# Performance work log

Measured on AMD Instinct MI355X. Metric: run time of the kernel, lower is better.

The kernel has to match this reference:

```python
import jax, jax.numpy as jnp
import numpy as np

N = 100_000      # total nodes in batched graph
NE = 800_000     # total edges
G = 1_000        # number of graphs in batch
V_DIM = 128      # node feat dim (== H_DIM, required by GRUCell usage)
E_DIM = 64       # edge feat dim
H_DIM = 128      # hidden dim
K_HEAD = 4       # multi-scale interaction heads


def _leaky(x):
    return jnp.where(x >= 0, x, 0.1 * x)


def _gru_cell(x, h, Wih, Whh, bih, bhh):
    # torch nn.GRUCell math; Wih/Whh stored as [in, 3*h] with (r,z,n) chunk order
    gi = x @ Wih + bih
    gh = h @ Whh + bhh
    ir, iz, inn = jnp.split(gi, 3, axis=-1)
    hr, hz, hn = jnp.split(gh, 3, axis=-1)
    r = jax.nn.sigmoid(ir + hr)
    z = jax.nn.sigmoid(iz + hz)
    n = jnp.tanh(inn + r * hn)
    return (1.0 - z) * n + z * h


def setup_inputs() -> dict:
    key = jax.random.key(0)
    ks = iter(jax.random.split(key, 48))
    def rn(shape, scale=0.05):
        return (jax.random.normal(next(ks), shape) * scale).astype(jnp.float32)
    inp = {}
    inp["v"] = rn((N, V_DIM), 1.0)
    inp["e"] = rn((NE, E_DIM), 1.0)
    inp["s"] = rn((G, V_DIM), 1.0)
    inp["edge_src"] = jax.random.randint(next(ks), (NE,), 0, N)
    inp["edge_dst"] = jax.random.randint(next(ks), (NE,), 0, N)
    inp["node_graph"] = jnp.repeat(jnp.arange(G), N // G)  # sorted segment ids
    # top-level linears (stored [in, out])
    inp["A_w"] = rn((V_DIM, H_DIM)); inp["A_b"] = rn((H_DIM,))
    inp["mA_w"] = rn((K_HEAD, V_DIM, H_DIM)); inp["mA_b"] = rn((K_HEAD, H_DIM))
    inp["mB_w"] = rn((K_HEAD, V_DIM, H_DIM)); inp["mB_b"] = rn((K_HEAD, H_DIM))
    inp["mC_w"] = rn((K_HEAD, H_DIM)); inp["mC_b"] = rn((K_HEAD,))
    inp["mD_w"] = rn((K_HEAD, V_DIM, H_DIM)); inp["mD_b"] = rn((K_HEAD, H_DIM))
    inp["B_w"] = rn((H_DIM * K_HEAD, H_DIM)); inp["B_b"] = rn((H_DIM,))
    inp["C_w"] = rn((V_DIM, H_DIM)); inp["C_b"] = rn((H_DIM,))
    inp["K_w"] = rn((E_DIM, H_DIM)); inp["K_b"] = rn((H_DIM,))
    inp["E_w"] = rn((H_DIM + V_DIM, H_DIM)); inp["E_b"] = rn((H_DIM,))
    for pfx in ("gm", "gs"):
        inp[pfx + "_A_w"] = rn((H_DIM, H_DIM)); inp[pfx + "_A_b"] = rn((H_DIM,))
        inp[pfx + "_B_w"] = rn((H_DIM, H_DIM)); inp[pfx + "_B_b"] = rn((H_DIM,))
        inp[pfx + "_Wih"] = rn((H_DIM, 3 * H_DIM)); inp[pfx + "_Whh"] = rn((H_DIM, 3 * H_DIM))
        inp[pfx + "_bih"] = rn((3 * H_DIM,)); inp[pfx + "_bhh"] = rn((3 * H_DIM,))
    return inp


def reference(v, e, s, edge_src, edge_dst, node_graph,
              A_w, A_b, mA_w, mA_b, mB_w, mB_b, mC_w, mC_b, mD_w, mD_b,
              B_w, B_b, C_w, C_b, K_w, K_b, E_w, E_b,
              gm_A_w, gm_A_b, gm_B_w, gm_B_b, gm_Wih, gm_Whh, gm_bih, gm_bhh,
              gs_A_w, gs_A_b, gs_B_w, gs_B_b, gs_Wih, gs_Whh, gs_bih, gs_bhh):
    # super -> super
    s2s = jnp.tanh(s @ A_w + A_b)                                       # [G,H]
    # multi-head node->super attention pooling (Multi_scale_interaction)
    d_node = jnp.tanh(jnp.einsum('nv,kvh->knh', v, mA_w) + mA_b[:, None, :])     # [K,N,H]
    d_super = jnp.tanh(jnp.einsum('gv,kvh->kgh', s, mB_w) + mB_b[:, None, :])    # [K,G,H]
    a = jnp.einsum('knh,kh->nk', d_node * d_super[:, node_graph, :], mC_w) + mC_b[None, :]  # [N,K]
    a_max = jax.ops.segment_max(a, node_graph, num_segments=G, indices_are_sorted=True)
    a_exp = jnp.exp(a - a_max[node_graph])
    denom = jax.ops.segment_sum(a_exp, node_graph, num_segments=G, indices_are_sorted=True)
    attn = a_exp / denom[node_graph]                                    # per-graph softmax, [N,K]
    d_v = jnp.einsum('nv,kvh->nkh', v, mD_w) + mD_b[None, :, :]         # [N,K,H]
    pooled = jax.ops.segment_sum(d_v * attn[:, :, None], node_graph, num_segments=G,
                                 indices_are_sorted=True)               # [G,K,H]
    m2s = jnp.tanh(pooled.reshape(G, K_HEAD * H_DIM) @ B_w + B_b)       # [G,H]
    # super -> node broadcast
    s2m = jnp.tanh(s @ C_w + C_b)[node_graph]                           # [N,H]
    # edge-wise message: leaky_relu(K(e) * v_src) summed into destination node
    ve = _leaky((e @ K_w + K_b) * v[edge_src])                          # [E,H]
    sve = jax.ops.segment_sum(ve, edge_dst, num_segments=N)             # [N,H]
    m2m = _leaky(jnp.concatenate([sve, v], axis=1) @ E_w + E_b)         # [N,H]
    # adaptive GRU gate: node update
    z_m = jax.nn.sigmoid(m2m @ gm_A_w + gm_A_b + s2m @ gm_B_w + gm_B_b)
    h_m = z_m * s2m + (1.0 - z_m) * m2m
    update_v = _gru_cell(v, h_m, gm_Wih, gm_Whh, gm_bih, gm_bhh)
    # adaptive GRU gate: supernode update
    z_s = jax.nn.sigmoid(s2s @ gs_A_w + gs_A_b + m2s @ gs_B_w + gs_B_b)
    h_s = z_s * m2s + (1.0 - z_s) * s2s
    update_s = _gru_cell(s, h_s, gs_Wih, gs_Whh, gs_bih, gs_bhh)
    return (update_v, update_s)
```

## Files before the change

### kernel.cpp

```cpp
#include <hip/hip_runtime.h>

#define NN   100000
#define NEDG 800000
#define NG   1000
#define HD   128
#define EDIM 64

typedef unsigned short u16;
typedef __bf16 bf16x8 __attribute__((ext_vector_type(8)));
typedef float f32x4 __attribute__((ext_vector_type(4)));
typedef u16 u16x8 __attribute__((ext_vector_type(8)));
typedef unsigned u32x4 __attribute__((ext_vector_type(4)));

#define MFMA16(a, b, c) __builtin_amdgcn_mfma_f32_16x16x32_bf16(a, b, c, 0, 0, 0)

#define WS_E    0
#define WS_GA   4096
#define WS_WIH  6144
#define WS_WHH  12288
#define WS_MA0  18432
#define WS_KW   26624
#define WS_LANES 27648

#define BF(base, NTT, ks, nt, lane) \
    (*(const bf16x8*)(wsw + (size_t)((base) + (((ks) * (NTT) + (nt)) * 64 + (lane))) * 8))

__device__ __forceinline__ float sigmoidf_(float x) { return 1.0f / (1.0f + __expf(-x)); }
__device__ __forceinline__ float tanhf_(float x) {
    float ax = fabsf(x);
    float e  = __expf(-2.0f * ax);
    float t  = (1.0f - e) / (1.0f + e);
    return copysignf(t, x);
}
__device__ __forceinline__ float leaky_(float x) { return x >= 0.f ? x : 0.1f * x; }
__device__ __forceinline__ u16 f2bf(float x) {
    union { float f; unsigned u; } c; c.f = x;
    unsigned r = c.u + 0x7FFF + ((c.u >> 16) & 1);
    return (u16)(r >> 16);
}
__device__ __forceinline__ float bfbits2f(unsigned hw) {
    union { unsigned u; float f; } c; c.u = hw << 16; return c.f;
}
__device__ __forceinline__ unsigned pack2bf(float lo, float hi) {
    return (unsigned)f2bf(lo) | ((unsigned)f2bf(hi) << 16);
}
__device__ __forceinline__ bf16x8 mk8(const float* __restrict__ p) {
    float4 a = *(const float4*)p;
    float4 b = *(const float4*)(p + 4);
    union { u32x4 u; bf16x8 v; } c;
    c.u[0] = pack2bf(a.x, a.y);
    c.u[1] = pack2bf(a.z, a.w);
    c.u[2] = pack2bf(b.x, b.y);
    c.u[3] = pack2bf(b.z, b.w);
    return c.v;
}

__device__ __forceinline__ void stg4(u16* lds, int P, int r, int c0, float4 v4) {
    int byteoff = (c0 << 1) ^ ((r & 7) << 4);
    u16* p = lds + r * P + (byteoff >> 1);
    p[0] = f2bf(v4.x); p[1] = f2bf(v4.y); p[2] = f2bf(v4.z); p[3] = f2bf(v4.w);
}
__device__ __forceinline__ void stg1(u16* lds, int P, int r, int c, u16 val) {
    int byteoff = (c << 1) ^ ((r & 7) << 4);
    lds[r * P + (byteoff >> 1)] = val;
}
__device__ __forceinline__ bf16x8 ldA(const u16* lds, int P, int r, int ks, int hi) {
    int byteoff = (ks * 64 + (hi << 4)) ^ ((r & 7) << 4);
    return *(const bf16x8*)(lds + r * P + (byteoff >> 1));
}

__global__ __launch_bounds__(256) void wconv(
    const float* __restrict__ E_w, const float* __restrict__ gmA_w,
    const float* __restrict__ Wih, const float* __restrict__ Whh,
    const float* __restrict__ mA_w, const float* __restrict__ K_w,
    u16* __restrict__ dst)
{
    int t = blockIdx.x * 256 + threadIdx.x;
    if (t >= WS_LANES) return;
    const float* W; int N; int local;
    if (t < 4096)       { W = E_w;  N = 128; local = t; }
    else if (t < 6144)  { W = gmA_w; N = 128; local = t - 4096; }
    else if (t < 12288) { W = Wih;  N = 384; local = t - 6144; }
    else if (t < 18432) { W = Whh;  N = 384; local = t - 12288; }
    else if (t < 26624) { int k = (t - 18432) >> 11; W = mA_w + k * 128 * 128; N = 128; local = (t - 18432) & 2047; }
    else                { W = K_w;  N = 128; local = t - 26624; }
    int lane = local & 63;
    int fid  = local >> 6;
    int NT = N >> 4;
    int ks = fid / NT, nt = fid - ks * NT;
    int krow = ks * 32 + ((lane >> 4) << 3);
    int col  = nt * 16 + (lane & 15);
    u16* d = dst + (size_t)t * 8;
    #pragma unroll
    for (int j = 0; j < 8; j++) d[j] = f2bf(W[(size_t)(krow + j) * N + col]);
}

__global__ __launch_bounds__(256) void k_hist(const int* __restrict__ edst, int* __restrict__ cnt) {
    int i = blockIdx.x * 256 + threadIdx.x;
    if (i < NEDG) atomicAdd(&cnt[edst[i]], 1);
}

__global__ __launch_bounds__(256) void k_scan1(const int* __restrict__ cnt,
                                               int* __restrict__ excl, int* __restrict__ bsum) {
    __shared__ int sd[256];
    int t = threadIdx.x, b = blockIdx.x;
    int base = b * 1024 + t * 4;
    int v0 = (base + 0 < NN) ? cnt[base + 0] : 0;
    int v1 = (base + 1 < NN) ? cnt[base + 1] : 0;
    int v2 = (base + 2 < NN) ? cnt[base + 2] : 0;
    int v3 = (base + 3 < NN) ? cnt[base + 3] : 0;
    int s = v0 + v1 + v2 + v3;
    sd[t] = s;
    __syncthreads();
    for (int off = 1; off < 256; off <<= 1) {
        int x = (t >= off) ? sd[t - off] : 0;
        __syncthreads();
        sd[t] += x;
        __syncthreads();
    }
    int incl = sd[t];
    int ex = incl - s;
    if (base + 0 < NN) excl[base + 0] = ex;
    if (base + 1 < NN) excl[base + 1] = ex + v0;
    if (base + 2 < NN) excl[base + 2] = ex + v0 + v1;
    if (base + 3 < NN) excl[base + 3] = ex + v0 + v1 + v2;
    if (t == 255) bsum[b] = incl;
}

#define NSCB 98
__global__ void k_scan2(int* __restrict__ bsum) {
    if (threadIdx.x == 0 && blockIdx.x == 0) {
        int run = 0;
        for (int i = 0; i < NSCB; i++) { int t = bsum[i]; bsum[i] = run; run += t; }
    }
}

__global__ __launch_bounds__(256) void k_scan3(const int* __restrict__ excl,
                                               const int* __restrict__ bsum,
                                               int* __restrict__ start) {
    int i = blockIdx.x * 256 + threadIdx.x;
    if (i < NN) start[i] = excl[i] + bsum[i >> 10];
}

__global__ __launch_bounds__(256) void k_scatter(const int* __restrict__ edst,
                                                 int* __restrict__ start,
                                                 int* __restrict__ perm) {
    int i = blockIdx.x * 256 + threadIdx.x;
    if (i < NEDG) {
        int pos = atomicAdd(&start[edst[i]], 1);
        perm[pos] = i;
    }
}

__global__ __launch_bounds__(128) void k1_graph(
    const float* __restrict__ s,
    const float* __restrict__ A_w, const float* __restrict__ A_b,
    const float* __restrict__ mB_w, const float* __restrict__ mB_b,
    const float* __restrict__ mC_w,
    const float* __restrict__ C_w, const float* __restrict__ C_b,
    const float* __restrict__ gmB_w, const float* __restrict__ gmA_b, const float* __restrict__ gmB_b,
    float* __restrict__ s2s, float* __restrict__ wkg,
    float* __restrict__ s2m_tab, float* __restrict__ t2)
{
    __shared__ float sm[HD];
    __shared__ float sm2[HD];
    const int g = blockIdx.x, t = threadIdx.x;
    sm[t] = s[g * HD + t];
    __syncthreads();
    {
        float a = 0.f;
        #pragma unroll 8
        for (int i = 0; i < HD; i++) a = fmaf(sm[i], A_w[i * HD + t], a);
        s2s[g * HD + t] = tanhf_(a + A_b[t]);
    }
    for (int k = 0; k < 4; k++) {
        float a = 0.f;
        const float* W = mB_w + k * HD * HD;
        #pragma unroll 8
        for (int i = 0; i < HD; i++) a = fmaf(sm[i], W[i * HD + t], a);
        float d = tanhf_(a + mB_b[k * HD + t]);
        wkg[(k * NG + g) * HD + t] = d * mC_w[k * HD + t];
    }
    float s2m;
    {
        float a = 0.f;
        #pragma unroll 8
        for (int i = 0; i < HD; i++) a = fmaf(sm[i], C_w[i * HD + t], a);
        s2m = tanhf_(a + C_b[t]);
        s2m_tab[g * HD + t] = s2m;
    }
    sm2[t] = s2m;
    __syncthreads();
    {
        float a = 0.f;
        #pragma unroll 8
        for (int i = 0; i < HD; i++) a = fmaf(sm2[i], gmB_w[i * HD + t], a);
        t2[g * HD + t] = a + gmA_b[t] + gmB_b[t];
    }
}

__global__ __launch_bounds__(256) void k2_ascore(
    const float* __restrict__ v, const int* __restrict__ ngr,
    const u16* __restrict__ wsw,
    const float* __restrict__ mA_b, const float* __restrict__ mC_b,
    const float* __restrict__ wkg,
    float* __restrict__ aexp, float* __restrict__ denom)
{
    __shared__ u16 VT[64 * 128];
    const int tid = threadIdx.x;
    const int n0 = blockIdx.x * 64;
    #pragma unroll
    for (int l = 0; l < 8; l++) {
        int i = tid + 256 * l;
        int r = i >> 5, c0 = (i & 31) << 2;
        int node = n0 + r;
        float4 vv = (node < NN) ? *(const float4*)(v + (size_t)node * HD + c0)
                                : make_float4(0.f, 0.f, 0.f, 0.f);
        stg4(VT, 128, r, c0, vv);
    }
    __syncthreads();
    const int lane = tid & 63, w = tid >> 6;
    const int l15 = lane & 15, hi = lane >> 4;
    const int rbase = w * 16;
    bf16x8 av[4];
    #pragma unroll
    for (int ks = 0; ks < 4; ks++) av[ks] = ldA(VT, 128, rbase + l15, ks, hi);
    int gq[4], nodeq[4];
    #pragma unroll
    for (int q = 0; q < 4; q++) {
        int nd = n0 + rbase + hi * 4 + q;
        nodeq[q] = nd;
        gq[q] = ngr[min(nd, NN - 1)];
    }
    for (int k = 0; k < 4; k++) {
        float rs[4] = {0.f, 0.f, 0.f, 0.f};
        const float* bias = mA_b + k * HD;
        #pragma unroll
        for (int nt = 0; nt < 8; nt++) {
            f32x4 acc = {0.f, 0.f, 0.f, 0.f};
            #pragma unroll
            for (int ks = 0; ks < 4; ks++)
                acc = MFMA16(av[ks], BF(WS_MA0 + k * 2048, 8, ks, nt, lane), acc);
            int col = nt * 16 + l15;
            float bb = bias[col];
            #pragma unroll
            for (int q = 0; q < 4; q++)
                rs[q] += tanhf_(acc[q] + bb) * wkg[((size_t)k * NG + gq[q]) * HD + col];
        }
        #pragma unroll
        for (int q = 0; q < 4; q++) {
            float x = rs[q];
            x += __shfl_xor(x, 1); x += __shfl_xor(x, 2);
            x += __shfl_xor(x, 4); x += __shfl_xor(x, 8);
            if (l15 == 0 && nodeq[q] < NN) {
                float ev = __expf(x + mC_b[k]);
                aexp[(size_t)nodeq[q] * 4 + k] = ev;
                atomicAdd(&denom[gq[q] * 4 + k], ev);
            }
        }
    }
}

#define OPW 66
__global__ __launch_bounds__(256) void k3_merge(
    const float* __restrict__ e, const float* __restrict__ v,
    const int* __restrict__ esrc, const int* __restrict__ edst,
    const int* __restrict__ perm,
    const u16* __restrict__ wsw, const float* __restrict__ K_b,
    float* __restrict__ sve)
{
    __shared__ u16 ET[64 * 64];
    __shared__ unsigned OUTP[64 * OPW];
    __shared__ int pid[64];
    __shared__ int dsta[64];
    const int tid = threadIdx.x;
    const int e0 = blockIdx.x * 64;
    if (tid < 64) {
        int p = perm[e0 + tid];
        pid[tid] = p;
        dsta[tid] = edst[p];
    }
    __syncthreads();
    #pragma unroll
    for (int l = 0; l < 4; l++) {
        int i = tid + 256 * l;
        int r = i >> 4, c0 = (i & 15) << 2;
        float4 ev4 = *(const float4*)(e + (size_t)pid[r] * EDIM + c0);
        stg4(ET, 64, r, c0, ev4);
    }
    __syncthreads();
    const int lane = tid & 63, w = tid >> 6;
    const int l15 = lane & 15, hi = lane >> 4;
    const int rbase = w * 16;
    bf16x8 ae[2];
    #pragma unroll
    for (int ks = 0; ks < 2; ks++) ae[ks] = ldA(ET, 64, rbase + l15, ks, hi);
    int sq[4];
    #pragma unroll
    for (int q = 0; q < 4; q++) sq[q] = esrc[pid[rbase + hi * 4 + q]];
    u16* OU = (u16*)OUTP;
    #pragma unroll
    for (int nt = 0; nt < 8; nt++) {
        f32x4 acc = {0.f, 0.f, 0.f, 0.f};
        acc = MFMA16(ae[0], BF(WS_KW, 8, 0, nt, lane), acc);
        acc = MFMA16(ae[1], BF(WS_KW, 8, 1, nt, lane), acc);
        int col = nt * 16 + l15;
        float kb = K_b[col];
        #pragma unroll
        for (int q = 0; q < 4; q++) {
            float val = leaky_((acc[q] + kb) * v[(size_t)sq[q] * HD + col]);
            OU[(rbase + hi * 4 + q) * (OPW * 2) + col] = f2bf(val);
        }
    }
    __syncthreads();
    {
        const int cp = tid & 63;
        const int qr = tid >> 6;
        const int r0 = qr * 16;
        int dcur = dsta[r0];
        unsigned x = OUTP[r0 * OPW + cp];
        float a0 = bfbits2f(x & 0xffff), a1 = bfbits2f(x >> 16);
        #pragma unroll
        for (int i = 1; i < 16; i++) {
            int r = r0 + i;
            int d = dsta[r];
            unsigned y = OUTP[r * OPW + cp];
            float y0 = bfbits2f(y & 0xffff), y1 = bfbits2f(y >> 16);
            if (d == dcur) { a0 += y0; a1 += y1; }
            else {
                atomicAdd(&sve[(size_t)dcur * HD + cp * 2 + 0], a0);
                atomicAdd(&sve[(size_t)dcur * HD + cp * 2 + 1], a1);
                dcur = d; a0 = y0; a1 = y1;
            }
        }
        atomicAdd(&sve[(size_t)dcur * HD + cp * 2 + 0], a0);
        atomicAdd(&sve[(size_t)dcur * HD + cp * 2 + 1], a1);
    }
}

__global__ __launch_bounds__(256) void k3_edge_unsorted(
    const float* __restrict__ e, const float* __restrict__ v,
    const int* __restrict__ esrc, const int* __restrict__ edst,
    const u16* __restrict__ wsw, const float* __restrict__ K_b,
    float* __restrict__ sve)
{
    __shared__ u16 ET[64 * 64];
    const int tid = threadIdx.x;
    const int e0 = blockIdx.x * 64;
    #pragma unroll
    for (int l = 0; l < 4; l++) {
        int i = tid + 256 * l;
        int r = i >> 4, c0 = (i & 15) << 2;
        float4 ev4 = *(const float4*)(e + (size_t)(e0 + r) * EDIM + c0);
        stg4(ET, 64, r, c0, ev4);
    }
    __syncthreads();
    const int lane = tid & 63, w = tid >> 6;
    const int l15 = lane & 15, hi = lane >> 4;
    const int rbase = w * 16;
    bf16x8 ae[2];
    #pragma unroll
    for (int ks = 0; ks < 2; ks++) ae[ks] = ldA(ET, 64, rbase + l15, ks, hi);
    int sq[4], dq[4];
    #pragma unroll
    for (int q = 0; q < 4; q++) {
        int ei = e0 + rbase + hi * 4 + q;
        sq[q] = esrc[ei]; dq[q] = edst[ei];
    }
    #pragma unroll
    for (int nt = 0; nt < 8; nt++) {
        f32x4 acc = {0.f, 0.f, 0.f, 0.f};
        acc = MFMA16(ae[0], BF(WS_KW, 8, 0, nt, lane), acc);
        acc = MFMA16(ae[1], BF(WS_KW, 8, 1, nt, lane), acc);
        int col = nt * 16 + l15;
        float kb = K_b[col];
        #pragma unroll
        for (int q = 0; q < 4; q++) {
            float val = leaky_((acc[q] + kb) * v[(size_t)sq[q] * HD + col]);
            atomicAdd(&sve[(size_t)dq[q] * HD + col], val);
        }
    }
}

__global__ __launch_bounds__(256) void k4_vbar(
    const float* __restrict__ v, const int* __restrict__ ngr,
    const float* __restrict__ aexp, const float* __restrict__ denom,
    float* __restrict__ vbar)
{
    const int tid = threadIdx.x;
    const int d = tid & 127;
    const int hf = tid >> 7;
    const int n0 = blockIdx.x * 32 + hf * 16;
    int gcur = -1;
    float a0 = 0.f, a1 = 0.f, a2 = 0.f, a3 = 0.f;
    float4 rd = make_float4(0.f, 0.f, 0.f, 0.f);
    for (int nd = 0; nd < 16; nd++) {
        int n = n0 + nd;
        int g = ngr[n];
        if (g != gcur) {
            if (gcur >= 0) {
                atomicAdd(&vbar[(gcur * 4 + 0) * HD + d], a0);
                atomicAdd(&vbar[(gcur * 4 + 1) * HD + d], a1);
                atomicAdd(&vbar[(gcur * 4 + 2) * HD + d], a2);
                atomicAdd(&vbar[(gcur * 4 + 3) * HD + d], a3);
                a0 = a1 = a2 = a3 = 0.f;
            }
            float4 dn = *(const float4*)&denom[g * 4];
            rd = make_float4(1.f / dn.x, 1.f / dn.y, 1.f / dn.z, 1.f / dn.w);
            gcur = g;
        }
        float4 ae = *(const float4*)&aexp[n * 4];
        float vv = v[(size_t)n * HD + d];
        a0 = fmaf(ae.x * rd.x, vv, a0);
        a1 = fmaf(ae.y * rd.y, vv, a1);
        a2 = fmaf(ae.z * rd.z, vv, a2);
        a3 = fmaf(ae.w * rd.w, vv, a3);
    }
    atomicAdd(&vbar[(gcur * 4 + 0) * HD + d], a0);
    atomicAdd(&vbar[(gcur * 4 + 1) * HD + d], a1);
    atomicAdd(&vbar[(gcur * 4 + 2) * HD + d], a2);
    atomicAdd(&vbar[(gcur * 4 + 3) * HD + d], a3);
}

__global__ __launch_bounds__(128) void k5_super(
    const float* __restrict__ s, const float* __restrict__ vbar,
    const float* __restrict__ mD_w, const float* __restrict__ mD_b,
    const float* __restrict__ B_w, const float* __restrict__ B_b,
    const float* __restrict__ s2s,
    const float* __restrict__ gsA_w, const float* __restrict__ gsA_b,
    const float* __restrict__ gsB_w, const float* __restrict__ gsB_b,
    const float* __restrict__ gsWih, const float* __restrict__ gsWhh,
    const float* __restrict__ gsbih, const float* __restrict__ gsbhh,
    float* __restrict__ out_s)
{
    __shared__ float vb[4 * HD];
    __shared__ float p[4 * HD];
    __shared__ float m2s_l[HD];
    __shared__ float s2s_l[HD];
    __shared__ float hs_l[HD];
    __shared__ float srow[HD];
    const int g = blockIdx.x, t = threadIdx.x;
    #pragma unroll
    for (int l = 0; l < 4; l++) vb[t + HD * l] = vbar[(size_t)g * 4 * HD + t + HD * l];
    srow[t]  = s[g * HD + t];
    s2s_l[t] = s2s[g * HD + t];
    __syncthreads();
    for (int k = 0; k < 4; k++) {
        float a = 0.f;
        const float* W = mD_w + k * HD * HD;
        #pragma unroll 8
        for (int i = 0; i < HD; i++) a = fmaf(vb[k * HD + i], W[i * HD + t], a);
        p[k * HD + t] = a + mD_b[k * HD + t];
    }
    __syncthreads();
    float m2s;
    {
        float a = 0.f;
        #pragma unroll 8
        for (int j = 0; j < 4 * HD; j++) a = fmaf(p[j], B_w[j * HD + t], a);
        m2s = tanhf_(a + B_b[t]);
        m2s_l[t] = m2s;
    }
    __syncthreads();
    float hs;
    {
        float za = 0.f, zb = 0.f;
        #pragma unroll 8
        for (int i = 0; i < HD; i++) {
            za = fmaf(s2s_l[i], gsA_w[i * HD + t], za);
            zb = fmaf(m2s_l[i], gsB_w[i * HD + t], zb);
        }
        float z = sigmoidf_(za + gsA_b[t] + zb + gsB_b[t]);
        hs = z * m2s + (1.f - z) * s2s_l[t];
        hs_l[t] = hs;
    }
    __syncthreads();
    float gi0 = 0.f, gh0 = 0.f, gi1 = 0.f, gh1 = 0.f, gi2 = 0.f, gh2 = 0.f;
    #pragma unroll 4
    for (int i = 0; i < HD; i++) {
        float sv = srow[i], hv = hs_l[i];
        gi0 = fmaf(sv, gsWih[i * 384 + t], gi0);
        gh0 = fmaf(hv, gsWhh[i * 384 + t], gh0);
        gi1 = fmaf(sv, gsWih[i * 384 + 128 + t], gi1);
        gh1 = fmaf(hv, gsWhh[i * 384 + 128 + t], gh1);
        gi2 = fmaf(sv, gsWih[i * 384 + 256 + t], gi2);
        gh2 = fmaf(hv, gsWhh[i * 384 + 256 + t], gh2);
    }
    float r  = sigmoidf_(gi0 + gsbih[t] + gh0 + gsbhh[t]);
    float z2 = sigmoidf_(gi1 + gsbih[128 + t] + gh1 + gsbhh[128 + t]);
    float nn = tanhf_(gi2 + gsbih[256 + t] + r * (gh2 + gsbhh[256 + t]));
    out_s[g * HD + t] = (1.f - z2) * nn + z2 * hs;
}

__global__ __launch_bounds__(256) void k6_node_sve(
    const float* __restrict__ v, const int* __restrict__ ngr,
    const float* __restrict__ sve, const u16* __restrict__ wsw,
    const float* __restrict__ E_b,
    const float* __restrict__ s2m_tab, const float* __restrict__ t2,
    const float* __restrict__ bih, const float* __restrict__ bhh,
    float* __restrict__ out_v)
{
    __shared__ u16 TT[4][16 * 128];
    const int tid = threadIdx.x;
    const int lane = tid & 63, w = tid >> 6;
    const int l15 = lane & 15, hi = lane >> 4;
    const int n0 = blockIdx.x * 64 + w * 16;
    u16* T = TT[w];
    const int arow = min(n0 + l15, NN - 1);
    bf16x8 av[4], ax[4];
    #pragma unroll
    for (int ks = 0; ks < 4; ks++) {
        av[ks] = mk8(v   + (size_t)arow * HD + ks * 32 + hi * 8);
        ax[ks] = mk8(sve + (size_t)arow * HD + ks * 32 + hi * 8);
    }
    int gq[4], nodeq[4];
    #pragma unroll
    for (int q = 0; q < 4; q++) {
        int nd = n0 + hi * 4 + q;
        nodeq[q] = nd;
        gq[q] = ngr[min(nd, NN - 1)];
    }
    unsigned m2mp[8][2];
    #pragma unroll
    for (int nt = 0; nt < 8; nt++) {
        f32x4 acc = {0.f, 0.f, 0.f, 0.f};
        #pragma unroll
        for (int ks = 0; ks < 4; ks++) acc = MFMA16(ax[ks], BF(WS_E, 8, ks, nt, lane), acc);
        #pragma unroll
        for (int ks = 0; ks < 4; ks++) acc = MFMA16(av[ks], BF(WS_E, 8, 4 + ks, nt, lane), acc);
        float eb = E_b[nt * 16 + l15];
        float m0 = leaky_(acc[0] + eb), m1 = leaky_(acc[1] + eb);
        float m2 = leaky_(acc[2] + eb), m3 = leaky_(acc[3] + eb);
        m2mp[nt][0] = pack2bf(m0, m1);
        m2mp[nt][1] = pack2bf(m2, m3);
        int col = nt * 16 + l15;
        stg1(T, 128, hi * 4 + 0, col, (u16)(m2mp[nt][0] & 0xffff));
        stg1(T, 128, hi * 4 + 1, col, (u16)(m2mp[nt][0] >> 16));
        stg1(T, 128, hi * 4 + 2, col, (u16)(m2mp[nt][1] & 0xffff));
        stg1(T, 128, hi * 4 + 3, col, (u16)(m2mp[nt][1] >> 16));
    }
    bf16x8 am[4];
    #pragma unroll
    for (int ks = 0; ks < 4; ks++) am[ks] = ldA(T, 128, l15, ks, hi);
    unsigned hmp[8][2];
    #pragma unroll
    for (int nt = 0; nt < 8; nt++) {
        f32x4 acc = {0.f, 0.f, 0.f, 0.f};
        #pragma unroll
        for (int ks = 0; ks < 4; ks++) acc = MFMA16(am[ks], BF(WS_GA, 8, ks, nt, lane), acc);
        int col = nt * 16 + l15;
        float m2mq[4] = { bfbits2f(m2mp[nt][0] & 0xffff), bfbits2f(m2mp[nt][0] >> 16),
                          bfbits2f(m2mp[nt][1] & 0xffff), bfbits2f(m2mp[nt][1] >> 16) };
        float hm[4];
        #pragma unroll
        for (int q = 0; q < 4; q++) {
            int g = gq[q];
            float z = sigmoidf_(acc[q] + t2[(size_t)g * HD + col]);
            hm[q] = z * s2m_tab[(size_t)g * HD + col] + (1.f - z) * m2mq[q];
        }
        hmp[nt][0] = pack2bf(hm[0], hm[1]);
        hmp[nt][1] = pack2bf(hm[2], hm[3]);
        stg1(T, 128, hi * 4 + 0, col, (u16)(hmp[nt][0] & 0xffff));
        stg1(T, 128, hi * 4 + 1, col, (u16)(hmp[nt][0] >> 16));
        stg1(T, 128, hi * 4 + 2, col, (u16)(hmp[nt][1] & 0xffff));
        stg1(T, 128, hi * 4 + 3, col, (u16)(hmp[nt][1] >> 16));
    }
    bf16x8 ah[4];
    #pragma unroll
    for (int ks = 0; ks < 4; ks++) ah[ks] = ldA(T, 128, l15, ks, hi);
    #pragma unroll
    for (int nt = 0; nt < 8; nt++) {
        f32x4 air = {0.f,0.f,0.f,0.f}, aiz = {0.f,0.f,0.f,0.f}, ain = {0.f,0.f,0.f,0.f};
        f32x4 ahr = {0.f,0.f,0.f,0.f}, ahz = {0.f,0.f,0.f,0.f}, ahn = {0.f,0.f,0.f,0.f};
        #pragma unroll
        for (int ks = 0; ks < 4; ks++) {
            air = MFMA16(av[ks], BF(WS_WIH, 24, ks, nt,      lane), air);
            ahr = MFMA16(ah[ks], BF(WS_WHH, 24, ks, nt,      lane), ahr);
            aiz = MFMA16(av[ks], BF(WS_WIH, 24, ks, nt + 8,  lane), aiz);
            ahz = MFMA16(ah[ks], BF(WS_WHH, 24, ks, nt + 8,  lane), ahz);
            ain = MFMA16(av[ks], BF(WS_WIH, 24, ks, nt + 16, lane), ain);
            ahn = MFMA16(ah[ks], BF(WS_WHH, 24, ks, nt + 16, lane), ahn);
        }
        int col = nt * 16 + l15;
        float br  = bih[col] + bhh[col];
        float bz  = bih[HD + col] + bhh[HD + col];
        float bi3 = bih[2 * HD + col];
        float bh3 = bhh[2 * HD + col];
        float hmq[4] = { bfbits2f(hmp[nt][0] & 0xffff), bfbits2f(hmp[nt][0] >> 16),
                         bfbits2f(hmp[nt][1] & 0xffff), bfbits2f(hmp[nt][1] >> 16) };
        #pragma unroll
        for (int q = 0; q < 4; q++) {
            float r   = sigmoidf_(air[q] + ahr[q] + br);
            float z   = sigmoidf_(aiz[q] + ahz[q] + bz);
            float nnv = tanhf_(ain[q] + bi3 + r * (ahn[q] + bh3));
            if (nodeq[q] < NN)
                out_v[(size_t)nodeq[q] * HD + col] = (1.f - z) * nnv + z * hmq[q];
        }
    }
}

extern "C" void kernel_launch(void* const* d_in, const int* in_sizes, int n_in,
                              void* d_out, int out_size, void* d_ws, size_t ws_size,
                              hipStream_t stream)
{
    const float* v    = (const float*)d_in[0];
    const float* e    = (const float*)d_in[1];
    const float* s    = (const float*)d_in[2];
    const int*   esrc = (const int*)d_in[3];
    const int*   edst = (const int*)d_in[4];
    const int*   ngr  = (const int*)d_in[5];
    const float* A_w  = (const float*)d_in[6];
    const float* A_b  = (const float*)d_in[7];
    const float* mA_w = (const float*)d_in[8];
    const float* mA_b = (const float*)d_in[9];
    const float* mB_w = (const float*)d_in[10];
    const float* mB_b = (const float*)d_in[11];
    const float* mC_w = (const float*)d_in[12];
    const float* mC_b = (const float*)d_in[13];
    const float* mD_w = (const float*)d_in[14];
    const float* mD_b = (const float*)d_in[15];
    const float* B_w  = (const float*)d_in[16];
    const float* B_b  = (const float*)d_in[17];
    const float* C_w  = (const float*)d_in[18];
    const float* C_b  = (const float*)d_in[19];
    const float* K_w  = (const float*)d_in[20];
    const float* K_b  = (const float*)d_in[21];
    const float* E_w  = (const float*)d_in[22];
    const float* E_b  = (const float*)d_in[23];
    const float* gmA_w = (const float*)d_in[24];
    const float* gmA_b = (const float*)d_in[25];
    const float* gmB_w = (const float*)d_in[26];
    const float* gmB_b = (const float*)d_in[27];
    const float* gmWih = (const float*)d_in[28];
    const float* gmWhh = (const float*)d_in[29];
    const float* gmbih = (const float*)d_in[30];
    const float* gmbhh = (const float*)d_in[31];
    const float* gsA_w = (const float*)d_in[32];
    const float* gsA_b = (const float*)d_in[33];
    const float* gsB_w = (const float*)d_in[34];
    const float* gsB_b = (const float*)d_in[35];
    const float* gsWih = (const float*)d_in[36];
    const float* gsWhh = (const float*)d_in[37];
    const float* gsbih = (const float*)d_in[38];
    const float* gsbhh = (const float*)d_in[39];

    float* ws      = (float*)d_ws;
    float* sve     = ws;
    float* aexp    = sve + 12800000;
    float* denom   = aexp + 400000;
    float* wkg     = denom + 4000;
    float* s2s     = wkg + 512000;
    float* s2m_tab = s2s + 128000;
    float* t2      = s2m_tab + 128000;
    float* vbar    = t2 + 128000;
    u16*   wswz    = (u16*)(vbar + 512000);
    int*   isc     = (int*)(wswz + 221184);
    int*   cnt     = isc;
    int*   excl    = cnt + 100000;
    int*   bsum    = excl + 100000;
    int*   startp  = bsum + 128;
    int*   perm    = startp + 100000;
    const size_t NEED_SORT = ((size_t)(perm + 800000 - (int*)d_ws)) * 4;
    const bool do_sort = ws_size >= NEED_SORT;

    hipMemsetAsync(sve, 0, (size_t)12800000 * 4, stream);
    hipMemsetAsync(denom, 0, (size_t)4000 * 4, stream);
    hipMemsetAsync(vbar, 0, (size_t)512000 * 4, stream);

    float* out_v = (float*)d_out;
    float* out_s = out_v + (size_t)NN * HD;

    wconv<<<(WS_LANES + 255) / 256, 256, 0, stream>>>(E_w, gmA_w, gmWih, gmWhh, mA_w, K_w, wswz);
    k1_graph<<<NG, 128, 0, stream>>>(s, A_w, A_b, mB_w, mB_b, mC_w, C_w, C_b,
                                     gmB_w, gmA_b, gmB_b, s2s, wkg, s2m_tab, t2);
    if (do_sort) {
        hipMemsetAsync(cnt, 0, (size_t)100000 * 4, stream);
        k_hist<<<(NEDG + 255) / 256, 256, 0, stream>>>(edst, cnt);
        k_scan1<<<NSCB, 256, 0, stream>>>(cnt, excl, bsum);
        k_scan2<<<1, 64, 0, stream>>>(bsum);
        k_scan3<<<(NN + 255) / 256, 256, 0, stream>>>(excl, bsum, startp);
        k_scatter<<<(NEDG + 255) / 256, 256, 0, stream>>>(edst, startp, perm);
    }
    k2_ascore<<<(NN + 63) / 64, 256, 0, stream>>>(v, ngr, wswz, mA_b, mC_b, wkg, aexp, denom);
    if (do_sort) {
        k3_merge<<<NEDG / 64, 256, 0, stream>>>(e, v, esrc, edst, perm, wswz, K_b, sve);
    } else {
        k3_edge_unsorted<<<NEDG / 64, 256, 0, stream>>>(e, v, esrc, edst, wswz, K_b, sve);
    }
    k4_vbar<<<NN / 32, 256, 0, stream>>>(v, ngr, aexp, denom, vbar);
    k5_super<<<NG, 128, 0, stream>>>(s, vbar, mD_w, mD_b, B_w, B_b, s2s,
                                     gsA_w, gsA_b, gsB_w, gsB_b,
                                     gsWih, gsWhh, gsbih, gsbhh, out_s);
    k6_node_sve<<<(NN + 63) / 64, 256, 0, stream>>>(v, ngr, sve, wswz, E_b, s2m_tab, t2,
                                                    gmbih, gmbhh, out_v);
}
```

Before: 718.8 us.

## Merge independent kernels into combined launches via block-index dispatch

Independent kernels are folded into shared launches that pick their work by block index. The edge merge (k3) and attention score (k2) share one grid, and the node GRU update (k6) and vbar pooling (k4) share another, with k5 moved after them. The aim is to cut launch gaps and let small, underfilled kernels overlap with large ones on idle compute units. In exchange the merged kernel uses the larger shared-memory footprint and register budget of the heavier body for every block, which may lower occupancy.

```diff
diff --git a/kernel.cpp b/kernel.cpp
--- a/kernel.cpp
+++ b/kernel.cpp
@@ -5,6 +5,11 @@
 #define NG   1000
 #define HD   128
 #define EDIM 64
+
+#define NB3 (NEDG / 64)
+#define NB2 ((NN + 63) / 64)
+#define NB6 ((NN + 63) / 64)
+#define NB4 (NN / 32)
 
 typedef unsigned short u16;
 typedef __bf16 bf16x8 __attribute__((ext_vector_type(8)));
@@ -199,16 +204,15 @@
     }
 }
 
-__global__ __launch_bounds__(256) void k2_ascore(
+__device__ __forceinline__ void k2_body(
+    int bid, int tid, u16* VT,
     const float* __restrict__ v, const int* __restrict__ ngr,
     const u16* __restrict__ wsw,
     const float* __restrict__ mA_b, const float* __restrict__ mC_b,
     const float* __restrict__ wkg,
     float* __restrict__ aexp, float* __restrict__ denom)
 {
-    __shared__ u16 VT[64 * 128];
-    const int tid = threadIdx.x;
-    const int n0 = blockIdx.x * 64;
+    const int n0 = bid * 64;
     #pragma unroll
     for (int l = 0; l < 8; l++) {
         int i = tid + 256 * l;
@@ -262,19 +266,19 @@
 }
 
 #define OPW 66
-__global__ __launch_bounds__(256) void k3_merge(
+__device__ __forceinline__ void k3_body(
+    int bid, int tid, char* SM,
     const float* __restrict__ e, const float* __restrict__ v,
     const int* __restrict__ esrc, const int* __restrict__ edst,
     const int* __restrict__ perm,
     const u16* __restrict__ wsw, const float* __restrict__ K_b,
     float* __restrict__ sve)
 {
-    __shared__ u16 ET[64 * 64];
-    __shared__ unsigned OUTP[64 * OPW];
-    __shared__ int pid[64];
-    __shared__ int dsta[64];
-    const int tid = threadIdx.x;
-    const int e0 = blockIdx.x * 64;
+    u16* ET = (u16*)SM;
+    unsigned* OUTP = (unsigned*)(SM + 8192);
+    int* pid = (int*)(SM + 8192 + 16896);
+    int* dsta = pid + 64;
+    const int e0 = bid * 64;
     if (tid < 64) {
         int p = perm[e0 + tid];
         pid[tid] = p;
@@ -338,6 +342,24 @@
     }
 }
 
+__global__ __launch_bounds__(256) void mega1(
+    const float* __restrict__ e, const float* __restrict__ v,
+    const int* __restrict__ esrc, const int* __restrict__ edst,
+    const int* __restrict__ perm, const int* __restrict__ ngr,
+    const u16* __restrict__ wsw, const float* __restrict__ K_b,
+    const float* __restrict__ mA_b, const float* __restrict__ mC_b,
+    const float* __restrict__ wkg,
+    float* __restrict__ sve, float* __restrict__ aexp, float* __restrict__ denom)
+{
+    __shared__ __align__(16) char SM[25600];
+    const int bid = blockIdx.x, tid = threadIdx.x;
+    if (bid < NB3) {
+        k3_body(bid, tid, SM, e, v, esrc, edst, perm, wsw, K_b, sve);
+    } else {
+        k2_body(bid - NB3, tid, (u16*)SM, v, ngr, wsw, mA_b, mC_b, wkg, aexp, denom);
+    }
+}
+
 __global__ __launch_bounds__(256) void k3_edge_unsorted(
     const float* __restrict__ e, const float* __restrict__ v,
     const int* __restrict__ esrc, const int* __restrict__ edst,
@@ -382,15 +404,26 @@
     }
 }
 
-__global__ __launch_bounds__(256) void k4_vbar(
+__global__ __launch_bounds__(256) void k2_standalone(
+    const float* __restrict__ v, const int* __restrict__ ngr,
+    const u16* __restrict__ wsw,
+    const float* __restrict__ mA_b, const float* __restrict__ mC_b,
+    const float* __restrict__ wkg,
+    float* __restrict__ aexp, float* __restrict__ denom)
+{
+    __shared__ u16 VT[64 * 128];
+    k2_body(blockIdx.x, threadIdx.x, VT, v, ngr, wsw, mA_b, mC_b, wkg, aexp, denom);
+}
+
+__device__ __forceinline__ void k4_body(
+    int bid, int tid,
     const float* __restrict__ v, const int* __restrict__ ngr,
     const float* __restrict__ aexp, const float* __restrict__ denom,
     float* __restrict__ vbar)
 {
-    const int tid = threadIdx.x;
     const int d = tid & 127;
     const int hf = tid >> 7;
-    const int n0 = blockIdx.x * 32 + hf * 16;
+    const int n0 = bid * 32 + hf * 16;
     int gcur = -1;
     float a0 = 0.f, a1 = 0.f, a2 = 0.f, a3 = 0.f;
     float4 rd = make_float4(0.f, 0.f, 0.f, 0.f);
@@ -422,77 +455,8 @@
     atomicAdd(&vbar[(gcur * 4 + 3) * HD + d], a3);
 }
 
-__global__ __launch_bounds__(128) void k5_super(
-    const float* __restrict__ s, const float* __restrict__ vbar,
-    const float* __restrict__ mD_w, const float* __restrict__ mD_b,
-    const float* __restrict__ B_w, const float* __restrict__ B_b,
-    const float* __restrict__ s2s,
-    const float* __restrict__ gsA_w, const float* __restrict__ gsA_b,
-    const float* __restrict__ gsB_w, const float* __restrict__ gsB_b,
-    const float* __restrict__ gsWih, const float* __restrict__ gsWhh,
-    const float* __restrict__ gsbih, const float* __restrict__ gsbhh,
-    float* __restrict__ out_s)
-{
-    __shared__ float vb[4 * HD];
-    __shared__ float p[4 * HD];
-    __shared__ float m2s_l[HD];
-    __shared__ float s2s_l[HD];
-    __shared__ float hs_l[HD];
-    __shared__ float srow[HD];
-    const int g = blockIdx.x, t = threadIdx.x;
-    #pragma unroll
-    for (int l = 0; l < 4; l++) vb[t + HD * l] = vbar[(size_t)g * 4 * HD + t + HD * l];
-    srow[t]  = s[g * HD + t];
-    s2s_l[t] = s2s[g * HD + t];
-    __syncthreads();
-    for (int k = 0; k < 4; k++) {
-        float a = 0.f;
-        const float* W = mD_w + k * HD * HD;
-        #pragma unroll 8
-        for (int i = 0; i < HD; i++) a = fmaf(vb[k * HD + i], W[i * HD + t], a);
-        p[k * HD + t] = a + mD_b[k * HD + t];
-    }
-    __syncthreads();
-    float m2s;
-    {
-        float a = 0.f;
-        #pragma unroll 8
-        for (int j = 0; j < 4 * HD; j++) a = fmaf(p[j], B_w[j * HD + t], a);
-        m2s = tanhf_(a + B_b[t]);
-        m2s_l[t] = m2s;
-    }
-    __syncthreads();
-    float hs;
-    {
-        float za = 0.f, zb = 0.f;
-        #pragma unroll 8
-        for (int i = 0; i < HD; i++) {
-            za = fmaf(s2s_l[i], gsA_w[i * HD + t], za);
-            zb = fmaf(m2s_l[i], gsB_w[i * HD + t], zb);
-        }
-        float z = sigmoidf_(za + gsA_b[t] + zb + gsB_b[t]);
-        hs = z * m2s + (1.f - z) * s2s_l[t];
-        hs_l[t] = hs;
-    }
-    __syncthreads();
-    float gi0 = 0.f, gh0 = 0.f, gi1 = 0.f, gh1 = 0.f, gi2 = 0.f, gh2 = 0.f;
-    #pragma unroll 4
-    for (int i = 0; i < HD; i++) {
-        float sv = srow[i], hv = hs_l[i];
-        gi0 = fmaf(sv, gsWih[i * 384 + t], gi0);
-        gh0 = fmaf(hv, gsWhh[i * 384 + t], gh0);
-        gi1 = fmaf(sv, gsWih[i * 384 + 128 + t], gi1);
-        gh1 = fmaf(hv, gsWhh[i * 384 + 128 + t], gh1);
-        gi2 = fmaf(sv, gsWih[i * 384 + 256 + t], gi2);
-        gh2 = fmaf(hv, gsWhh[i * 384 + 256 + t], gh2);
-    }
-    float r  = sigmoidf_(gi0 + gsbih[t] + gh0 + gsbhh[t]);
-    float z2 = sigmoidf_(gi1 + gsbih[128 + t] + gh1 + gsbhh[128 + t]);
-    float nn = tanhf_(gi2 + gsbih[256 + t] + r * (gh2 + gsbhh[256 + t]));
-    out_s[g * HD + t] = (1.f - z2) * nn + z2 * hs;
-}
-
-__global__ __launch_bounds__(256) void k6_node_sve(
+__device__ __forceinline__ void k6_body(
+    int bid, int tid, u16* T,
     const float* __restrict__ v, const int* __restrict__ ngr,
     const float* __restrict__ sve, const u16* __restrict__ wsw,
     const float* __restrict__ E_b,
@@ -500,12 +464,9 @@
     const float* __restrict__ bih, const float* __restrict__ bhh,
     float* __restrict__ out_v)
 {
-    __shared__ u16 TT[4][16 * 128];
-    const int tid = threadIdx.x;
-    const int lane = tid & 63, w = tid >> 6;
+    const int lane = tid & 63;
     const int l15 = lane & 15, hi = lane >> 4;
-    const int n0 = blockIdx.x * 64 + w * 16;
-    u16* T = TT[w];
+    const int n0 = bid * 64 + (tid >> 6) * 16;
     const int arow = min(n0 + l15, NN - 1);
     bf16x8 av[4], ax[4];
     #pragma unroll
@@ -597,6 +558,94 @@
                 out_v[(size_t)nodeq[q] * HD + col] = (1.f - z) * nnv + z * hmq[q];
         }
     }
+}
+
+__global__ __launch_bounds__(256) void mega2(
+    const float* __restrict__ v, const int* __restrict__ ngr,
+    const float* __restrict__ sve, const u16* __restrict__ wsw,
+    const float* __restrict__ E_b,
+    const float* __restrict__ s2m_tab, const float* __restrict__ t2,
+    const float* __restrict__ bih, const float* __restrict__ bhh,
+    const float* __restrict__ aexp, const float* __restrict__ denom,
+    float* __restrict__ out_v, float* __restrict__ vbar)
+{
+    __shared__ u16 TT[4][16 * 128];
+    const int bid = blockIdx.x, tid = threadIdx.x;
+    if (bid < NB6) {
+        k6_body(bid, tid, TT[tid >> 6], v, ngr, sve, wsw, E_b, s2m_tab, t2, bih, bhh, out_v);
+    } else {
+        k4_body(bid - NB6, tid, v, ngr, aexp, denom, vbar);
+    }
+}
+
+__global__ __launch_bounds__(128) void k5_super(
+    const float* __restrict__ s, const float* __restrict__ vbar,
+    const float* __restrict__ mD_w, const float* __restrict__ mD_b,
+    const float* __restrict__ B_w, const float* __restrict__ B_b,
+    const float* __restrict__ s2s,
+    const float* __restrict__ gsA_w, const float* __restrict__ gsA_b,
+    const float* __restrict__ gsB_w, const float* __restrict__ gsB_b,
+    const float* __restrict__ gsWih, const float* __restrict__ gsWhh,
+    const float* __restrict__ gsbih, const float* __restrict__ gsbhh,
+    float* __restrict__ out_s)
+{
+    __shared__ float vb[4 * HD];
+    __shared__ float p[4 * HD];
+    __shared__ float m2s_l[HD];
+    __shared__ float s2s_l[HD];
+    __shared__ float hs_l[HD];
+    __shared__ float srow[HD];
+    const int g = blockIdx.x, t = threadIdx.x;
+    #pragma unroll
+    for (int l = 0; l < 4; l++) vb[t + HD * l] = vbar[(size_t)g * 4 * HD + t + HD * l];
+    srow[t]  = s[g * HD + t];
+    s2s_l[t] = s2s[g * HD + t];
+    __syncthreads();
+    for (int k = 0; k < 4; k++) {
+        float a = 0.f;
+        const float* W = mD_w + k * HD * HD;
+        #pragma unroll 8
+        for (int i = 0; i < HD; i++) a = fmaf(vb[k * HD + i], W[i * HD + t], a);
+        p[k * HD + t] = a + mD_b[k * HD + t];
+    }
+    __syncthreads();
+    float m2s;
+    {
+        float a = 0.f;
+        #pragma unroll 8
+        for (int j = 0; j < 4 * HD; j++) a = fmaf(p[j], B_w[j * HD + t], a);
+        m2s = tanhf_(a + B_b[t]);
+        m2s_l[t] = m2s;
+    }
+    __syncthreads();
+    float hs;
+    {
+        float za = 0.f, zb = 0.f;
+        #pragma unroll 8
+        for (int i = 0; i < HD; i++) {
+            za = fmaf(s2s_l[i], gsA_w[i * HD + t], za);
+            zb = fmaf(m2s_l[i], gsB_w[i * HD + t], zb);
+        }
+        float z = sigmoidf_(za + gsA_b[t] + zb + gsB_b[t]);
+        hs = z * m2s + (1.f - z) * s2s_l[t];
+        hs_l[t] = hs;
+    }
+    __syncthreads();
+    float gi0 = 0.f, gh0 = 0.f, gi1 = 0.f, gh1 = 0.f, gi2 = 0.f, gh2 = 0.f;
+    #pragma unroll 4
+    for (int i = 0; i < HD; i++) {
+        float sv = srow[i], hv = hs_l[i];
+        gi0 = fmaf(sv, gsWih[i * 384 + t], gi0);
+        gh0 = fmaf(hv, gsWhh[i * 384 + t], gh0);
+        gi1 = fmaf(sv, gsWih[i * 384 + 128 + t], gi1);
+        gh1 = fmaf(hv, gsWhh[i * 384 + 128 + t], gh1);
+        gi2 = fmaf(sv, gsWih[i * 384 + 256 + t], gi2);
+        gh2 = fmaf(hv, gsWhh[i * 384 + 256 + t], gh2);
+    }
+    float r  = sigmoidf_(gi0 + gsbih[t] + gh0 + gsbhh[t]);
+    float z2 = sigmoidf_(gi1 + gsbih[128 + t] + gh1 + gsbhh[128 + t]);
+    float nn = tanhf_(gi2 + gsbih[256 + t] + r * (gh2 + gsbhh[256 + t]));
+    out_s[g * HD + t] = (1.f - z2) * nn + z2 * hs;
 }
 
 extern "C" void kernel_launch(void* const* d_in, const int* in_sizes, int n_in,
@@ -680,17 +729,15 @@
         k_scan2<<<1, 64, 0, stream>>>(bsum);
         k_scan3<<<(NN + 255) / 256, 256, 0, stream>>>(excl, bsum, startp);
         k_scatter<<<(NEDG + 255) / 256, 256, 0, stream>>>(edst, startp, perm);
-    }
-    k2_ascore<<<(NN + 63) / 64, 256, 0, stream>>>(v, ngr, wswz, mA_b, mC_b, wkg, aexp, denom);
-    if (do_sort) {
-        k3_merge<<<NEDG / 64, 256, 0, stream>>>(e, v, esrc, edst, perm, wswz, K_b, sve);
+        mega1<<<NB3 + NB2, 256, 0, stream>>>(e, v, esrc, edst, perm, ngr, wswz, K_b,
+                                             mA_b, mC_b, wkg, sve, aexp, denom);
     } else {
+        k2_standalone<<<NB2, 256, 0, stream>>>(v, ngr, wswz, mA_b, mC_b, wkg, aexp, denom);
         k3_edge_unsorted<<<NEDG / 64, 256, 0, stream>>>(e, v, esrc, edst, wswz, K_b, sve);
     }
-    k4_vbar<<<NN / 32, 256, 0, stream>>>(v, ngr, aexp, denom, vbar);
+    mega2<<<NB6 + NB4, 256, 0, stream>>>(v, ngr, sve, wswz, E_b, s2m_tab, t2,
+                                         gmbih, gmbhh, aexp, denom, out_v, vbar);
     k5_super<<<NG, 128, 0, stream>>>(s, vbar, mD_w, mD_b, B_w, B_b, s2s,
                                      gsA_w, gsA_b, gsB_w, gsB_b,
                                      gsWih, gsWhh, gsbih, gsbhh, out_s);
-    k6_node_sve<<<(NN + 63) / 64, 256, 0, stream>>>(v, ngr, sve, wswz, E_b, s2m_tab, t2,
-                                                    gmbih, gmbhh, out_v);
-}
+}
```

New measurement: 710.9 us. No clear change (-1.1%).
